# Kernel tuning notes

Hardware: AMD Instinct MI355X
Metric: run time of the kernel (lower is better)

Reference implementation:

```python
import jax, jax.numpy as jnp
import numpy as np

T, B, D = 2048, 8, 1024
INIT_ALPHA_BIAS = 2.0


def setup_inputs() -> dict:
    key = jax.random.key(0)
    k1, k2, k3, k4 = jax.random.split(key, 4)
    xav = float(np.sqrt(6.0 / (D + D)))  # xavier_uniform bound
    return {
        "x": jax.random.normal(k1, (T, B, D), dtype=jnp.float32),
        "h0": jax.random.normal(k2, (B, D), dtype=jnp.float32),
        "W_alpha": jax.random.uniform(k3, (D, D), jnp.float32, -xav, xav),
        "b_alpha": jnp.full((D,), INIT_ALPHA_BIAS, dtype=jnp.float32),
        "W_v": jax.random.uniform(k4, (D, D), jnp.float32, -xav, xav),
        "b_v": jnp.zeros((D,), dtype=jnp.float32),
    }


def reference(x, h0, W_alpha, b_alpha, W_v, b_v):
    # Gates/values for all timesteps at once (batched GEMMs): [T, B, D]
    alpha = jax.nn.sigmoid(jnp.einsum("tbd,ed->tbe", x, W_alpha) + b_alpha)
    v = jnp.einsum("tbd,ed->tbe", x, W_v) + b_v

    def step(h_prev, av):
        a_t, v_t = av
        h_new = a_t * h_prev + (1.0 - a_t) * v_t
        out_t = h_new * jax.nn.silu(h_new)
        return h_new, (h_new, out_t)

    _, (hs, output) = jax.lax.scan(step, h0, (alpha, v))
    h = jnp.concatenate([h0[None], hs], axis=0)  # [T+1, B, D]
    return output, h
```

## Files before the change

kernel.cpp:

```cpp
#include <hip/hip_runtime.h>
#include <hip/hip_bf16.h>

#define T_DIM 2048
#define B_DIM 8
#define D_DIM 1024
#define M_DIM (T_DIM * B_DIM)
#define K_DIM D_DIM
#define NW_DIM (2 * D_DIM)
#define NCH (B_DIM * D_DIM)
#define NCH4 (NCH / 4)
#define CHUNKS 64
#define CHUNK_LEN 32

typedef __attribute__((ext_vector_type(8))) short bf16x8;
typedef __attribute__((ext_vector_type(4))) float f32x4;

__device__ __forceinline__ unsigned short bf16_rne(float f) {
    unsigned u = __float_as_uint(f);
    unsigned r = u + 0x7fffu + ((u >> 16) & 1u);
    return (unsigned short)(r >> 16);
}

__device__ __forceinline__ float sigmoidf(float z) {
    return 1.0f / (1.0f + __expf(-z));
}

__device__ __forceinline__ void decode_av(unsigned u, float& a, float& v) {
    a = (float)(u & 0xffffu) * (1.0f / 65535.f);
    v = __uint_as_float(u & 0xffff0000u);
}

__device__ __forceinline__ void load_lds16(const void* g, void* l) {
    __builtin_amdgcn_global_load_lds(
        (const __attribute__((address_space(1))) void*)g,
        (__attribute__((address_space(3))) void*)l,
        16, 0, 0);
}

__global__ __launch_bounds__(256) void convert_all_kernel(
    const float4* __restrict__ x,
    const float4* __restrict__ Wa,
    const float4* __restrict__ Wv,
    ushort4* __restrict__ xb,
    ushort4* __restrict__ Wcat) {
    const int nx4 = M_DIM * K_DIM / 4;
    const int half4 = D_DIM * D_DIM / 4;
    int i = blockIdx.x * 256 + threadIdx.x;
    float4 f;
    ushort4* __restrict__ dst;
    int di;
    if (i < nx4) {
        f = x[i];
        dst = xb;
        di = i;
    } else {
        int j = i - nx4;
        f = (j < half4) ? Wa[j] : Wv[j - half4];
        dst = Wcat;
        di = j;
    }
    ushort4 o;
    o.x = bf16_rne(f.x);
    o.y = bf16_rne(f.y);
    o.z = bf16_rne(f.z);
    o.w = bf16_rne(f.w);
    dst[di] = o;
}

__global__ __launch_bounds__(512, 4) void gemm_fused_kernel(
    const unsigned short* __restrict__ A,
    const unsigned short* __restrict__ W,
    const float* __restrict__ ba,
    const float* __restrict__ bv,
    unsigned short* __restrict__ av) {
    extern __shared__ __attribute__((aligned(16))) char smem[];

    const int tid = threadIdx.x;
    const int lane = tid & 63;
    const int w = tid >> 6;
    const int wm = w >> 2;
    const int wn = w & 3;
    const int quad = lane >> 4;
    const int l16 = lane & 15;

    const int bid = blockIdx.x;
    const int swz = (bid & 7) * 128 + (bid >> 3);
    const int bx = swz & 7;
    const int by = swz >> 3;
    const int bm = by * 128;
    const int bn = bx * 256;

    const int vsw = (((l16 & 1) << 2) | quad) ^ (l16 >> 1);
    const int rdA = wm * 4096 + (l16 >> 1) * 128 + vsw * 16;
    const int rdB = wn * 4096 + (l16 >> 1) * 128 + vsw * 16;

    const int hl = lane >> 3;
    const int vp = (lane & 7) ^ hl;
    const int qsrc = vp & 3;
    const int rb = (vp >> 2) & 1;
    const int rA  = 16 * w + 2 * hl + rb;
    const int rB0 = 32 * w + 2 * hl + rb;
    const int rB1 = rB0 + 16;
    const char* Ab = (const char*)A;
    const char* Wb = (const char*)W;
    const size_t offA  = (size_t)(bm + rA ) * 2048 + (size_t)qsrc * 16;
    const size_t offB0 = (size_t)(bn + rB0) * 2048 + (size_t)qsrc * 16;
    const size_t offB1 = (size_t)(bn + rB1) * 2048 + (size_t)qsrc * 16;
    const int ldsA  = w * 1024;
    const int ldsB0 = (2 * w) * 1024;
    const int ldsB1 = (2 * w + 1) * 1024;

    f32x4 acc[4][4];
    {
        f32x4 zero = {0.f, 0.f, 0.f, 0.f};
#pragma unroll
        for (int i = 0; i < 4; ++i)
#pragma unroll
            for (int j = 0; j < 4; ++j) acc[i][j] = zero;
    }

    auto stage = [&](int buf, int t) {
        char* bA = smem + buf * 24576;
        char* bB = bA + 8192;
        const size_t ko = (size_t)t * 64;
        load_lds16(Ab + offA + ko, bA + ldsA);
        load_lds16(Wb + offB0 + ko, bB + ldsB0);
        load_lds16(Wb + offB1 + ko, bB + ldsB1);
    };

    auto tile_step = [&](int buf, int nbuf, int tn, bool do_stage, int vm,
                         bool bar) {
        const char* bA = smem + buf * 24576;
        const char* bB = bA + 8192;
        bf16x8 af[4], bfr[4];
#pragma unroll
        for (int i = 0; i < 4; ++i)
            af[i] = *(const bf16x8*)(bA + rdA + i * 1024);
#pragma unroll
        for (int j = 0; j < 4; ++j)
            bfr[j] = *(const bf16x8*)(bB + rdB + j * 1024);
        if (do_stage) stage(nbuf, tn);
        asm volatile("s_waitcnt lgkmcnt(0)" ::: "memory");
        __builtin_amdgcn_sched_barrier(0);
        __builtin_amdgcn_s_setprio(1);
#pragma unroll
        for (int i = 0; i < 4; ++i)
#pragma unroll
            for (int j = 0; j < 4; ++j)
                acc[i][j] = __builtin_amdgcn_mfma_f32_16x16x32_bf16(
                    af[i], bfr[j], acc[i][j], 0, 0, 0);
        __builtin_amdgcn_s_setprio(0);
        if (vm == 3) asm volatile("s_waitcnt vmcnt(3)" ::: "memory");
        else if (vm == 0) asm volatile("s_waitcnt vmcnt(0)" ::: "memory");
        if (bar) __builtin_amdgcn_s_barrier();
    };

    stage(0, 0);
    stage(1, 1);
    asm volatile("s_waitcnt vmcnt(3)" ::: "memory");
    __builtin_amdgcn_s_barrier();

    for (int it = 0; it < 10; ++it) {
        const int t = it * 3;
        tile_step(0, 2, t + 2, true, 3, true);
        tile_step(1, 0, t + 3, true, 3, true);
        tile_step(2, 1, t + 4, true, 3, true);
    }
    tile_step(0, 0, 0, false, 0, true);
    tile_step(1, 0, 0, false, -1, false);

    const bool is_alpha = (bn < D_DIM);
    const float* __restrict__ bias = is_alpha ? ba : bv;
    const int nb = bn - (is_alpha ? 0 : D_DIM);
    const int sel = is_alpha ? 0 : 1;
#pragma unroll
    for (int j = 0; j < 4; ++j) {
        const int n = nb + wn * 64 + j * 16 + l16;
        const float bias_n = bias[n];
#pragma unroll
        for (int i = 0; i < 4; ++i) {
            const int m0 = bm + wm * 64 + i * 16 + quad * 4;
#pragma unroll
            for (int r = 0; r < 4; ++r) {
                float val = acc[i][j][r] + bias_n;
                unsigned short s;
                if (is_alpha)
                    s = (unsigned short)(sigmoidf(val) * 65535.f + 0.5f);
                else
                    s = bf16_rne(val);
                av[((size_t)(m0 + r) * D_DIM + n) * 2 + sel] = s;
            }
        }
    }
}


__global__ __launch_bounds__(256) void scan_phase1_kernel(
    const uint4* __restrict__ av,
    float4* __restrict__ P,
    float4* __restrict__ Q) {
    const int j4 = blockIdx.x * 256 + threadIdx.x;
    const int c = blockIdx.y;
    float4 Pr = {1.f, 1.f, 1.f, 1.f};
    float4 Qr = {0.f, 0.f, 0.f, 0.f};
    size_t base = (size_t)c * CHUNK_LEN * NCH4 + j4;
#pragma unroll 4
    for (int t = 0; t < CHUNK_LEN; ++t) {
        uint4 u = av[base + (size_t)t * NCH4];
        float a0, v0, a1, v1, a2, v2, a3, v3;
        decode_av(u.x, a0, v0);
        decode_av(u.y, a1, v1);
        decode_av(u.z, a2, v2);
        decode_av(u.w, a3, v3);
        Pr.x *= a0; Pr.y *= a1; Pr.z *= a2; Pr.w *= a3;
        Qr.x = a0 * Qr.x + (1.f - a0) * v0;
        Qr.y = a1 * Qr.y + (1.f - a1) * v1;
        Qr.z = a2 * Qr.z + (1.f - a2) * v2;
        Qr.w = a3 * Qr.w + (1.f - a3) * v3;
    }
    P[(size_t)c * NCH4 + j4] = Pr;
    Q[(size_t)c * NCH4 + j4] = Qr;
}

__global__ __launch_bounds__(256) void scan_phase2_kernel(
    const float* __restrict__ P, const float* __restrict__ Q,
    const float* __restrict__ h0,
    float* __restrict__ Hc,
    float* __restrict__ hbase) {
    const int ch = blockIdx.x * 256 + threadIdx.x;
    float h = h0[ch];
    hbase[ch] = h;
#pragma unroll 8
    for (int c = 0; c < CHUNKS; ++c) {
        Hc[(size_t)c * NCH + ch] = h;
        h = P[(size_t)c * NCH + ch] * h + Q[(size_t)c * NCH + ch];
    }
}

__global__ __launch_bounds__(256) void scan_phase3_kernel(
    uint4* __restrict__ av_out,
    float4* __restrict__ hout,
    const float4* __restrict__ Hc) {
    const int j4 = blockIdx.x * 256 + threadIdx.x;
    const int c = blockIdx.y;
    float4 h = Hc[(size_t)c * NCH4 + j4];
    size_t base = (size_t)c * CHUNK_LEN * NCH4 + j4;
#pragma unroll 4
    for (int t = 0; t < CHUNK_LEN; ++t) {
        uint4 u = av_out[base + (size_t)t * NCH4];
        float a0, v0, a1, v1, a2, v2, a3, v3;
        decode_av(u.x, a0, v0);
        decode_av(u.y, a1, v1);
        decode_av(u.z, a2, v2);
        decode_av(u.w, a3, v3);
        h.x = a0 * h.x + (1.f - a0) * v0;
        h.y = a1 * h.y + (1.f - a1) * v1;
        h.z = a2 * h.z + (1.f - a2) * v2;
        h.w = a3 * h.w + (1.f - a3) * v3;
        uint4 o;
        o.x = __float_as_uint(h.x * h.x * sigmoidf(h.x));
        o.y = __float_as_uint(h.y * h.y * sigmoidf(h.y));
        o.z = __float_as_uint(h.z * h.z * sigmoidf(h.z));
        o.w = __float_as_uint(h.w * h.w * sigmoidf(h.w));
        av_out[base + (size_t)t * NCH4] = o;
        hout[((size_t)c * CHUNK_LEN + t + 1) * NCH4 + j4] = h;
    }
}

extern "C" void kernel_launch(void* const* d_in, const int* in_sizes, int n_in,
                              void* d_out, int out_size, void* d_ws, size_t ws_size,
                              hipStream_t stream) {
    const float* x  = (const float*)d_in[0];
    const float* h0 = (const float*)d_in[1];
    const float* Wa = (const float*)d_in[2];
    const float* ba = (const float*)d_in[3];
    const float* Wv = (const float*)d_in[4];
    const float* bv = (const float*)d_in[5];

    float* out = (float*)d_out;
    float* hbase = out + (size_t)T_DIM * NCH;
    unsigned short* av = (unsigned short*)out;

    char* ws = (char*)d_ws;
    unsigned short* xb   = (unsigned short*)ws;
    unsigned short* Wcat = (unsigned short*)(ws + 33554432);
    float* P  = (float*)(ws + 37748736);
    float* Q  = (float*)(ws + 39845888);
    float* Hc = (float*)(ws + 41943040);

    static bool attr_done = false;
    if (!attr_done) {
        hipFuncSetAttribute(reinterpret_cast<const void*>(gemm_fused_kernel),
                            hipFuncAttributeMaxDynamicSharedMemorySize, 73728);
        attr_done = true;
    }

    const int nconv = (M_DIM * K_DIM / 4) + (2 * D_DIM * D_DIM / 4);
    convert_all_kernel<<<nconv / 256, 256, 0, stream>>>(
        (const float4*)x, (const float4*)Wa, (const float4*)Wv,
        (ushort4*)xb, (ushort4*)Wcat);

    gemm_fused_kernel<<<1024, 512, 73728, stream>>>(xb, Wcat, ba, bv, av);

    dim3 sgrid(NCH4 / 256, CHUNKS);
    scan_phase1_kernel<<<sgrid, 256, 0, stream>>>(
        (const uint4*)out, (float4*)P, (float4*)Q);
    scan_phase2_kernel<<<NCH / 256, 256, 0, stream>>>(
        P, Q, h0, Hc, hbase);
    scan_phase3_kernel<<<sgrid, 256, 0, stream>>>(
        (uint4*)out, (float4*)hbase, (const float4*)Hc);
}
```

Baseline: 305.3 us.

## Fuse three scan phases into one cooperative kernel and grid-stride conversion

Merges the three chunked-scan kernels into a single cooperative kernel of 512 blocks that uses grid.sync barriers between phases. The goal is to remove two kernel launch gaps and the tail drain between dependent phases. The conversion kernel also becomes a grid-stride loop over 2048 blocks instead of one thread per float4. In exchange, the serial phase 2 now runs on only 32 of the 512 blocks while the rest wait at the barrier, and the grid-wide syncs have their own cost.

Measured after the change: 527.3 us. 72.7% more time.

```diff
diff --git a/kernel.cpp b/kernel.cpp
--- a/kernel.cpp
+++ b/kernel.cpp
@@ -1,5 +1,8 @@
 #include <hip/hip_runtime.h>
 #include <hip/hip_bf16.h>
+#include <hip/hip_cooperative_groups.h>
+
+namespace cg = cooperative_groups;
 
 #define T_DIM 2048
 #define B_DIM 8
@@ -45,26 +48,29 @@
     ushort4* __restrict__ Wcat) {
     const int nx4 = M_DIM * K_DIM / 4;
     const int half4 = D_DIM * D_DIM / 4;
-    int i = blockIdx.x * 256 + threadIdx.x;
-    float4 f;
-    ushort4* __restrict__ dst;
-    int di;
-    if (i < nx4) {
-        f = x[i];
-        dst = xb;
-        di = i;
-    } else {
-        int j = i - nx4;
-        f = (j < half4) ? Wa[j] : Wv[j - half4];
-        dst = Wcat;
-        di = j;
-    }
-    ushort4 o;
-    o.x = bf16_rne(f.x);
-    o.y = bf16_rne(f.y);
-    o.z = bf16_rne(f.z);
-    o.w = bf16_rne(f.w);
-    dst[di] = o;
+    const int ntot = nx4 + 2 * half4;
+#pragma unroll 2
+    for (int i = blockIdx.x * 256 + threadIdx.x; i < ntot; i += 2048 * 256) {
+        float4 f;
+        ushort4* __restrict__ dst;
+        int di;
+        if (i < nx4) {
+            f = x[i];
+            dst = xb;
+            di = i;
+        } else {
+            int j = i - nx4;
+            f = (j < half4) ? Wa[j] : Wv[j - half4];
+            dst = Wcat;
+            di = j;
+        }
+        ushort4 o;
+        o.x = bf16_rne(f.x);
+        o.y = bf16_rne(f.y);
+        o.z = bf16_rne(f.z);
+        o.w = bf16_rne(f.w);
+        dst[di] = o;
+    }
 }
 
 __global__ __launch_bounds__(512, 4) void gemm_fused_kernel(
@@ -194,76 +200,83 @@
     }
 }
 
-
-__global__ __launch_bounds__(256) void scan_phase1_kernel(
-    const uint4* __restrict__ av,
-    float4* __restrict__ P,
-    float4* __restrict__ Q) {
-    const int j4 = blockIdx.x * 256 + threadIdx.x;
-    const int c = blockIdx.y;
-    float4 Pr = {1.f, 1.f, 1.f, 1.f};
-    float4 Qr = {0.f, 0.f, 0.f, 0.f};
-    size_t base = (size_t)c * CHUNK_LEN * NCH4 + j4;
+__global__ __launch_bounds__(256) void scan_fused_kernel(
+    uint4* __restrict__ av,
+    float* __restrict__ hbase,
+    const float* __restrict__ h0,
+    float* __restrict__ Pg,
+    float* __restrict__ Qg,
+    float* __restrict__ Hcg) {
+    cg::grid_group grid = cg::this_grid();
+    const int tid = threadIdx.x;
+    const int bxg = blockIdx.x & 7;
+    const int c   = blockIdx.x >> 3;
+    const int j4  = bxg * 256 + tid;
+    float4* P4  = (float4*)Pg;
+    float4* Q4  = (float4*)Qg;
+    float4* Hc4 = (float4*)Hcg;
+
+    {
+        float4 Pr = {1.f, 1.f, 1.f, 1.f};
+        float4 Qr = {0.f, 0.f, 0.f, 0.f};
+        size_t base = (size_t)c * CHUNK_LEN * NCH4 + j4;
 #pragma unroll 4
-    for (int t = 0; t < CHUNK_LEN; ++t) {
-        uint4 u = av[base + (size_t)t * NCH4];
-        float a0, v0, a1, v1, a2, v2, a3, v3;
-        decode_av(u.x, a0, v0);
-        decode_av(u.y, a1, v1);
-        decode_av(u.z, a2, v2);
-        decode_av(u.w, a3, v3);
-        Pr.x *= a0; Pr.y *= a1; Pr.z *= a2; Pr.w *= a3;
-        Qr.x = a0 * Qr.x + (1.f - a0) * v0;
-        Qr.y = a1 * Qr.y + (1.f - a1) * v1;
-        Qr.z = a2 * Qr.z + (1.f - a2) * v2;
-        Qr.w = a3 * Qr.w + (1.f - a3) * v3;
-    }
-    P[(size_t)c * NCH4 + j4] = Pr;
-    Q[(size_t)c * NCH4 + j4] = Qr;
-}
-
-__global__ __launch_bounds__(256) void scan_phase2_kernel(
-    const float* __restrict__ P, const float* __restrict__ Q,
-    const float* __restrict__ h0,
-    float* __restrict__ Hc,
-    float* __restrict__ hbase) {
-    const int ch = blockIdx.x * 256 + threadIdx.x;
-    float h = h0[ch];
-    hbase[ch] = h;
+        for (int t = 0; t < CHUNK_LEN; ++t) {
+            uint4 u = av[base + (size_t)t * NCH4];
+            float a0, v0, a1, v1, a2, v2, a3, v3;
+            decode_av(u.x, a0, v0);
+            decode_av(u.y, a1, v1);
+            decode_av(u.z, a2, v2);
+            decode_av(u.w, a3, v3);
+            Pr.x *= a0; Pr.y *= a1; Pr.z *= a2; Pr.w *= a3;
+            Qr.x = a0 * Qr.x + (1.f - a0) * v0;
+            Qr.y = a1 * Qr.y + (1.f - a1) * v1;
+            Qr.z = a2 * Qr.z + (1.f - a2) * v2;
+            Qr.w = a3 * Qr.w + (1.f - a3) * v3;
+        }
+        P4[(size_t)c * NCH4 + j4] = Pr;
+        Q4[(size_t)c * NCH4 + j4] = Qr;
+    }
+    __threadfence();
+    grid.sync();
+
+    if (blockIdx.x < NCH / 256) {
+        const int ch = blockIdx.x * 256 + tid;
+        float h = h0[ch];
+        hbase[ch] = h;
 #pragma unroll 8
-    for (int c = 0; c < CHUNKS; ++c) {
-        Hc[(size_t)c * NCH + ch] = h;
-        h = P[(size_t)c * NCH + ch] * h + Q[(size_t)c * NCH + ch];
-    }
-}
-
-__global__ __launch_bounds__(256) void scan_phase3_kernel(
-    uint4* __restrict__ av_out,
-    float4* __restrict__ hout,
-    const float4* __restrict__ Hc) {
-    const int j4 = blockIdx.x * 256 + threadIdx.x;
-    const int c = blockIdx.y;
-    float4 h = Hc[(size_t)c * NCH4 + j4];
-    size_t base = (size_t)c * CHUNK_LEN * NCH4 + j4;
+        for (int cc = 0; cc < CHUNKS; ++cc) {
+            Hcg[(size_t)cc * NCH + ch] = h;
+            h = Pg[(size_t)cc * NCH + ch] * h + Qg[(size_t)cc * NCH + ch];
+        }
+    }
+    __threadfence();
+    grid.sync();
+
+    {
+        float4 h = Hc4[(size_t)c * NCH4 + j4];
+        float4* hout = (float4*)hbase;
+        size_t base = (size_t)c * CHUNK_LEN * NCH4 + j4;
 #pragma unroll 4
-    for (int t = 0; t < CHUNK_LEN; ++t) {
-        uint4 u = av_out[base + (size_t)t * NCH4];
-        float a0, v0, a1, v1, a2, v2, a3, v3;
-        decode_av(u.x, a0, v0);
-        decode_av(u.y, a1, v1);
-        decode_av(u.z, a2, v2);
-        decode_av(u.w, a3, v3);
-        h.x = a0 * h.x + (1.f - a0) * v0;
-        h.y = a1 * h.y + (1.f - a1) * v1;
-        h.z = a2 * h.z + (1.f - a2) * v2;
-        h.w = a3 * h.w + (1.f - a3) * v3;
-        uint4 o;
-        o.x = __float_as_uint(h.x * h.x * sigmoidf(h.x));
-        o.y = __float_as_uint(h.y * h.y * sigmoidf(h.y));
-        o.z = __float_as_uint(h.z * h.z * sigmoidf(h.z));
-        o.w = __float_as_uint(h.w * h.w * sigmoidf(h.w));
-        av_out[base + (size_t)t * NCH4] = o;
-        hout[((size_t)c * CHUNK_LEN + t + 1) * NCH4 + j4] = h;
+        for (int t = 0; t < CHUNK_LEN; ++t) {
+            uint4 u = av[base + (size_t)t * NCH4];
+            float a0, v0, a1, v1, a2, v2, a3, v3;
+            decode_av(u.x, a0, v0);
+            decode_av(u.y, a1, v1);
+            decode_av(u.z, a2, v2);
+            decode_av(u.w, a3, v3);
+            h.x = a0 * h.x + (1.f - a0) * v0;
+            h.y = a1 * h.y + (1.f - a1) * v1;
+            h.z = a2 * h.z + (1.f - a2) * v2;
+            h.w = a3 * h.w + (1.f - a3) * v3;
+            uint4 o;
+            o.x = __float_as_uint(h.x * h.x * sigmoidf(h.x));
+            o.y = __float_as_uint(h.y * h.y * sigmoidf(h.y));
+            o.z = __float_as_uint(h.z * h.z * sigmoidf(h.z));
+            o.w = __float_as_uint(h.w * h.w * sigmoidf(h.w));
+            av[base + (size_t)t * NCH4] = o;
+            hout[((size_t)c * CHUNK_LEN + t + 1) * NCH4 + j4] = h;
+        }
     }
 }
 
@@ -295,18 +308,15 @@
         attr_done = true;
     }
 
-    const int nconv = (M_DIM * K_DIM / 4) + (2 * D_DIM * D_DIM / 4);
-    convert_all_kernel<<<nconv / 256, 256, 0, stream>>>(
+    convert_all_kernel<<<2048, 256, 0, stream>>>(
         (const float4*)x, (const float4*)Wa, (const float4*)Wv,
         (ushort4*)xb, (ushort4*)Wcat);
 
     gemm_fused_kernel<<<1024, 512, 73728, stream>>>(xb, Wcat, ba, bv, av);
 
-    dim3 sgrid(NCH4 / 256, CHUNKS);
-    scan_phase1_kernel<<<sgrid, 256, 0, stream>>>(
-        (const uint4*)out, (float4*)P, (float4*)Q);
-    scan_phase2_kernel<<<NCH / 256, 256, 0, stream>>>(
-        P, Q, h0, Hc, hbase);
-    scan_phase3_kernel<<<sgrid, 256, 0, stream>>>(
-        (uint4*)out, (float4*)hbase, (const float4*)Hc);
-}
+    uint4* av4 = (uint4*)out;
+    void* sargs[] = {(void*)&av4, (void*)&hbase, (void*)&h0,
+                     (void*)&P, (void*)&Q, (void*)&Hc};
+    hipLaunchCooperativeKernel((const void*)scan_fused_kernel,
+                               dim3(512), dim3(256), sargs, 0, stream);
+}
```

## Use finer scan chunks with hierarchical fold/expand and grid-stride conversion

Applied to the files above, without the earlier changes.

The chunked scan now uses 256 chunks of length 8 instead of 64 of length 32, so phases 1 and 3 run four times as many blocks with shorter serial loops. Two new kernels reduce the 256 chunk summaries to 64 and expand the 64 chunk-start states back to 256, which keeps the sequential phase-2 loop at 64 steps. The scan scratch buffers now reuse the start of the workspace, which is safe only because xb is dead once the GEMM finishes. The conversion kernel also switches to a fixed 2048-block grid-stride loop. The trade-off is two extra launches and extra P/Q/H traffic in exchange for more parallelism in the memory-bound scan phases.

After: 318.1 us. 1.04x slower.

```diff
diff --git a/kernel.cpp b/kernel.cpp
--- a/kernel.cpp
+++ b/kernel.cpp
@@ -6,11 +6,12 @@
 #define D_DIM 1024
 #define M_DIM (T_DIM * B_DIM)
 #define K_DIM D_DIM
-#define NW_DIM (2 * D_DIM)
 #define NCH (B_DIM * D_DIM)
 #define NCH4 (NCH / 4)
-#define CHUNKS 64
-#define CHUNK_LEN 32
+#define CHUNKS 256
+#define CHUNK_LEN 8
+#define CCHUNKS 64
+#define CSUB 4
 
 typedef __attribute__((ext_vector_type(8))) short bf16x8;
 typedef __attribute__((ext_vector_type(4))) float f32x4;
@@ -45,26 +46,29 @@
     ushort4* __restrict__ Wcat) {
     const int nx4 = M_DIM * K_DIM / 4;
     const int half4 = D_DIM * D_DIM / 4;
-    int i = blockIdx.x * 256 + threadIdx.x;
-    float4 f;
-    ushort4* __restrict__ dst;
-    int di;
-    if (i < nx4) {
-        f = x[i];
-        dst = xb;
-        di = i;
-    } else {
-        int j = i - nx4;
-        f = (j < half4) ? Wa[j] : Wv[j - half4];
-        dst = Wcat;
-        di = j;
-    }
-    ushort4 o;
-    o.x = bf16_rne(f.x);
-    o.y = bf16_rne(f.y);
-    o.z = bf16_rne(f.z);
-    o.w = bf16_rne(f.w);
-    dst[di] = o;
+    const int ntot = nx4 + 2 * half4;
+#pragma unroll 2
+    for (int i = blockIdx.x * 256 + threadIdx.x; i < ntot; i += 2048 * 256) {
+        float4 f;
+        ushort4* __restrict__ dst;
+        int di;
+        if (i < nx4) {
+            f = x[i];
+            dst = xb;
+            di = i;
+        } else {
+            int j = i - nx4;
+            f = (j < half4) ? Wa[j] : Wv[j - half4];
+            dst = Wcat;
+            di = j;
+        }
+        ushort4 o;
+        o.x = bf16_rne(f.x);
+        o.y = bf16_rne(f.y);
+        o.z = bf16_rne(f.z);
+        o.w = bf16_rne(f.w);
+        dst[di] = o;
+    }
 }
 
 __global__ __launch_bounds__(512, 4) void gemm_fused_kernel(
@@ -204,7 +208,7 @@
     float4 Pr = {1.f, 1.f, 1.f, 1.f};
     float4 Qr = {0.f, 0.f, 0.f, 0.f};
     size_t base = (size_t)c * CHUNK_LEN * NCH4 + j4;
-#pragma unroll 4
+#pragma unroll
     for (int t = 0; t < CHUNK_LEN; ++t) {
         uint4 u = av[base + (size_t)t * NCH4];
         float a0, v0, a1, v1, a2, v2, a3, v3;
@@ -222,30 +226,70 @@
     Q[(size_t)c * NCH4 + j4] = Qr;
 }
 
+__global__ __launch_bounds__(256) void scan_fold_kernel(
+    const float4* __restrict__ P256, const float4* __restrict__ Q256,
+    float4* __restrict__ P64, float4* __restrict__ Q64) {
+    const int j4 = blockIdx.x * 256 + threadIdx.x;
+    const int cc = blockIdx.y;
+    float4 P = {1.f, 1.f, 1.f, 1.f};
+    float4 Q = {0.f, 0.f, 0.f, 0.f};
+#pragma unroll
+    for (int s = 0; s < CSUB; ++s) {
+        size_t idx = (size_t)(CSUB * cc + s) * NCH4 + j4;
+        float4 Ps = P256[idx];
+        float4 Qs = Q256[idx];
+        Q.x = Ps.x * Q.x + Qs.x;  P.x *= Ps.x;
+        Q.y = Ps.y * Q.y + Qs.y;  P.y *= Ps.y;
+        Q.z = Ps.z * Q.z + Qs.z;  P.z *= Ps.z;
+        Q.w = Ps.w * Q.w + Qs.w;  P.w *= Ps.w;
+    }
+    P64[(size_t)cc * NCH4 + j4] = P;
+    Q64[(size_t)cc * NCH4 + j4] = Q;
+}
+
 __global__ __launch_bounds__(256) void scan_phase2_kernel(
-    const float* __restrict__ P, const float* __restrict__ Q,
+    const float* __restrict__ P64, const float* __restrict__ Q64,
     const float* __restrict__ h0,
-    float* __restrict__ Hc,
+    float* __restrict__ Hc64,
     float* __restrict__ hbase) {
     const int ch = blockIdx.x * 256 + threadIdx.x;
     float h = h0[ch];
     hbase[ch] = h;
 #pragma unroll 8
-    for (int c = 0; c < CHUNKS; ++c) {
-        Hc[(size_t)c * NCH + ch] = h;
-        h = P[(size_t)c * NCH + ch] * h + Q[(size_t)c * NCH + ch];
+    for (int cc = 0; cc < CCHUNKS; ++cc) {
+        Hc64[(size_t)cc * NCH + ch] = h;
+        h = P64[(size_t)cc * NCH + ch] * h + Q64[(size_t)cc * NCH + ch];
+    }
+}
+
+__global__ __launch_bounds__(256) void scan_expand_kernel(
+    const float4* __restrict__ P256, const float4* __restrict__ Q256,
+    const float4* __restrict__ Hc64, float4* __restrict__ Hc256) {
+    const int j4 = blockIdx.x * 256 + threadIdx.x;
+    const int cc = blockIdx.y;
+    float4 h = Hc64[(size_t)cc * NCH4 + j4];
+#pragma unroll
+    for (int s = 0; s < CSUB; ++s) {
+        size_t idx = (size_t)(CSUB * cc + s) * NCH4 + j4;
+        Hc256[idx] = h;
+        float4 Ps = P256[idx];
+        float4 Qs = Q256[idx];
+        h.x = Ps.x * h.x + Qs.x;
+        h.y = Ps.y * h.y + Qs.y;
+        h.z = Ps.z * h.z + Qs.z;
+        h.w = Ps.w * h.w + Qs.w;
     }
 }
 
 __global__ __launch_bounds__(256) void scan_phase3_kernel(
     uint4* __restrict__ av_out,
     float4* __restrict__ hout,
-    const float4* __restrict__ Hc) {
+    const float4* __restrict__ Hc256) {
     const int j4 = blockIdx.x * 256 + threadIdx.x;
     const int c = blockIdx.y;
-    float4 h = Hc[(size_t)c * NCH4 + j4];
+    float4 h = Hc256[(size_t)c * NCH4 + j4];
     size_t base = (size_t)c * CHUNK_LEN * NCH4 + j4;
-#pragma unroll 4
+#pragma unroll
     for (int t = 0; t < CHUNK_LEN; ++t) {
         uint4 u = av_out[base + (size_t)t * NCH4];
         float a0, v0, a1, v1, a2, v2, a3, v3;
@@ -284,9 +328,12 @@
     char* ws = (char*)d_ws;
     unsigned short* xb   = (unsigned short*)ws;
     unsigned short* Wcat = (unsigned short*)(ws + 33554432);
-    float* P  = (float*)(ws + 37748736);
-    float* Q  = (float*)(ws + 39845888);
-    float* Hc = (float*)(ws + 41943040);
+    float* P256  = (float*)(ws + 0);
+    float* Q256  = (float*)(ws + 8388608);
+    float* Hc256 = (float*)(ws + 16777216);
+    float* P64   = (float*)(ws + 25165824);
+    float* Q64   = (float*)(ws + 27262976);
+    float* Hc64  = (float*)(ws + 29360128);
 
     static bool attr_done = false;
     if (!attr_done) {
@@ -295,18 +342,23 @@
         attr_done = true;
     }
 
-    const int nconv = (M_DIM * K_DIM / 4) + (2 * D_DIM * D_DIM / 4);
-    convert_all_kernel<<<nconv / 256, 256, 0, stream>>>(
+    convert_all_kernel<<<2048, 256, 0, stream>>>(
         (const float4*)x, (const float4*)Wa, (const float4*)Wv,
         (ushort4*)xb, (ushort4*)Wcat);
 
     gemm_fused_kernel<<<1024, 512, 73728, stream>>>(xb, Wcat, ba, bv, av);
 
-    dim3 sgrid(NCH4 / 256, CHUNKS);
-    scan_phase1_kernel<<<sgrid, 256, 0, stream>>>(
-        (const uint4*)out, (float4*)P, (float4*)Q);
+    dim3 fgrid(NCH4 / 256, CHUNKS);
+    dim3 cgrid(NCH4 / 256, CCHUNKS);
+    scan_phase1_kernel<<<fgrid, 256, 0, stream>>>(
+        (const uint4*)out, (float4*)P256, (float4*)Q256);
+    scan_fold_kernel<<<cgrid, 256, 0, stream>>>(
+        (const float4*)P256, (const float4*)Q256, (float4*)P64, (float4*)Q64);
     scan_phase2_kernel<<<NCH / 256, 256, 0, stream>>>(
-        P, Q, h0, Hc, hbase);
-    scan_phase3_kernel<<<sgrid, 256, 0, stream>>>(
-        (uint4*)out, (float4*)hbase, (const float4*)Hc);
-}
+        P64, Q64, h0, Hc64, hbase);
+    scan_expand_kernel<<<cgrid, 256, 0, stream>>>(
+        (const float4*)P256, (const float4*)Q256, (const float4*)Hc64,
+        (float4*)Hc256);
+    scan_phase3_kernel<<<fgrid, 256, 0, stream>>>(
+        (uint4*)out, (float4*)hbase, (const float4*)Hc256);
+}
```
